# Performance work log

Measured on AMD Instinct MI355X. Metric: run time of the kernel, lower is better.

The kernel has to match this reference:

```python
import jax, jax.numpy as jnp
import numpy as np

C_Z = 128
C_H = 128
N = 768
B = 1
EPS = 1e-5


def _layer_norm(x, w, b):
    m = jnp.mean(x, axis=-1, keepdims=True)
    v = jnp.mean(jnp.square(x - m), axis=-1, keepdims=True)
    return (x - m) * jax.lax.rsqrt(v + EPS) * w + b


def setup_inputs() -> dict:
    key = jax.random.key(0)
    ks = jax.random.split(key, 12)
    s_z = 1.0 / np.sqrt(C_Z)
    s_h = 1.0 / np.sqrt(C_H)
    return {
        "z": jax.random.normal(ks[0], (B, N, N, C_Z), dtype=jnp.float32),
        "mask": jnp.ones((B, N, N), dtype=jnp.float32),
        "norm_in_weight": jnp.ones((C_Z,), dtype=jnp.float32),
        "norm_in_bias": jnp.zeros((C_Z,), dtype=jnp.float32),
        "ab_p_weight": jax.random.normal(ks[1], (2 * C_H, C_Z), dtype=jnp.float32) * s_z,
        "ab_p_bias": jnp.zeros((2 * C_H,), dtype=jnp.float32),
        "ab_g_weight": jax.random.normal(ks[2], (2 * C_H, C_Z), dtype=jnp.float32) * s_z,
        "ab_g_bias": jnp.zeros((2 * C_H,), dtype=jnp.float32),
        "g_weight": jax.random.normal(ks[3], (C_Z, C_Z), dtype=jnp.float32) * s_z,
        "g_bias": jnp.ones((C_Z,), dtype=jnp.float32),
        "norm_out_weight": jnp.ones((C_H,), dtype=jnp.float32),
        "norm_out_bias": jnp.zeros((C_H,), dtype=jnp.float32),
        "z_weight": jax.random.normal(ks[4], (C_Z, C_H), dtype=jnp.float32) * s_h,
        "z_bias": jnp.zeros((C_Z,), dtype=jnp.float32),
    }


def reference(z, mask, norm_in_weight, norm_in_bias, ab_p_weight, ab_p_bias,
              ab_g_weight, ab_g_bias, g_weight, g_bias,
              norm_out_weight, norm_out_bias, z_weight, z_bias):
    # z: [B, N, N, c_z]; mask: [B, N, N]
    zn = _layer_norm(z, norm_in_weight, norm_in_bias)
    # fused gated projection: p * sigmoid(g), masked
    p = jnp.einsum('bijc,dc->bijd', zn, ab_p_weight) + ab_p_bias
    g = jax.nn.sigmoid(jnp.einsum('bijc,dc->bijd', zn, ab_g_weight) + ab_g_bias)
    ab = p * g * mask[..., None]  # [B, N, N, 2*c_h]
    a, b = ab[..., :C_H], ab[..., C_H:]
    # outgoing triangle multiplication: sum over k of a_ik * b_jk
    x = jnp.einsum('bikc,bjkc->bijc', a, b)  # [B, N, N, c_h]
    x = _layer_norm(x, norm_out_weight, norm_out_bias)
    x = jnp.einsum('bijc,dc->bijd', x, z_weight) + z_bias  # [B, N, N, c_z]
    gate = jax.nn.sigmoid(jnp.einsum('bijc,dc->bijd', zn, g_weight) + g_bias)
    return x * gate
```

## Files before the change

### kernel.cpp

```cpp
#include <hip/hip_runtime.h>

typedef unsigned short ushort_t;
typedef __attribute__((ext_vector_type(4))) unsigned short u16x4;
typedef __attribute__((ext_vector_type(8))) unsigned short u16x8;
typedef __attribute__((ext_vector_type(2))) unsigned short u16x2;
typedef __attribute__((ext_vector_type(4))) float f32x4;
typedef __attribute__((ext_vector_type(8))) __bf16 bf16x8;

constexpr int N_ = 768;
constexpr int NN = N_ * N_;
constexpr int C  = 128;

__device__ __forceinline__ unsigned short f2bf(float f) {
  union { float f; unsigned int u; } v; v.f = f;
  unsigned int r = v.u + 0x7fffu + ((v.u >> 16) & 1u);
  return (unsigned short)(r >> 16);
}
__device__ __forceinline__ float bf2f(unsigned short u) {
  union { unsigned int i; float f; } v; v.i = ((unsigned int)u) << 16;
  return v.f;
}
__device__ __forceinline__ float sigm(float x) { return 1.f / (1.f + __expf(-x)); }

__device__ __forceinline__ void gload16(const void* g, void* l) {
  __builtin_amdgcn_global_load_lds(
      (const __attribute__((address_space(1))) unsigned int*)g,
      (__attribute__((address_space(3))) unsigned int*)l, 16, 0, 0);
}

__global__ __launch_bounds__(256) void k1_ln(const float* __restrict__ z,
                                             const float* __restrict__ w,
                                             const float* __restrict__ b,
                                             ushort_t* __restrict__ zn) {
  int row  = blockIdx.x * 4 + (threadIdx.x >> 6);
  int lane = threadIdx.x & 63;
  const float* src = z + (size_t)row * C;
  float2 v = *(const float2*)(src + lane * 2);
  float sm = v.x + v.y;
#pragma unroll
  for (int m = 1; m < 64; m <<= 1) sm += __shfl_xor(sm, m);
  float mean = sm * (1.f / 128.f);
  float d0 = v.x - mean, d1 = v.y - mean;
  float sq = d0 * d0 + d1 * d1;
#pragma unroll
  for (int m = 1; m < 64; m <<= 1) sq += __shfl_xor(sq, m);
  float rstd = rsqrtf(sq * (1.f / 128.f) + 1e-5f);
  float2 wv = *(const float2*)(w + lane * 2);
  float2 bv = *(const float2*)(b + lane * 2);
  u16x2 o; o.x = f2bf(d0 * rstd * wv.x + bv.x); o.y = f2bf(d1 * rstd * wv.y + bv.y);
  *(u16x2*)(zn + (size_t)row * C + lane * 2) = o;
}

__global__ void k0_cvt(const float* __restrict__ zw, const float* __restrict__ Wp,
                       const float* __restrict__ Wg, const float* __restrict__ Wgate,
                       ushort_t* __restrict__ zwb, ushort_t* __restrict__ Wall) {
  int i = blockIdx.x * 256 + threadIdx.x;
  if (i < 16384) zwb[i] = f2bf(zw[i]);
  if (i < 81920) {
    float v = (i < 32768) ? Wp[i] : (i < 65536 ? Wg[i - 32768] : Wgate[i - 65536]);
    Wall[i] = f2bf(v);
  }
}

constexpr int K2_ZN  = 0;
constexpr int K2_WB0 = 32768;
constexpr int K2_WB1 = 49152;
__global__ __launch_bounds__(256, 2) void k2_proj(
    const ushort_t* __restrict__ zn, const ushort_t* __restrict__ Wall,
    const float* __restrict__ bp, const float* __restrict__ bg,
    const float* __restrict__ bgate, const float* __restrict__ mask,
    ushort_t* __restrict__ a_t, ushort_t* __restrict__ b_t,
    ushort_t* __restrict__ gate_t) {
  __shared__ __align__(16) char smem[65536];
  int ij0 = blockIdx.x * 128;
  int t = threadIdx.x, lane = t & 63, wid = t >> 6;
  int rl = lane & 15, gq = lane >> 4;

  auto stage_wb = [&](int wrowbase, int wboff) {
#pragma unroll
    for (int pass = 0; pass < 4; ++pass) {
      int idx = pass * 256 + t;
      int row = idx >> 4, slot = idx & 15;
      int gcol = (slot * 16) ^ ((row & 7) << 4);
      gload16((const char*)Wall + (size_t)(wrowbase + row) * 256 + gcol,
              smem + wboff + idx * 16);
    }
  };

  {
    const char* base = (const char*)(zn + (size_t)ij0 * C);
#pragma unroll
    for (int iss = 0; iss < 8; ++iss) {
      int idx = iss * 256 + t;
      int row = idx >> 4, slot = idx & 15;
      int gcol = (slot * 16) ^ ((row & 7) << 4);
      gload16(base + row * 256 + gcol, smem + K2_ZN + idx * 16);
    }
  }
  stage_wb(0, K2_WB0);
  stage_wb(256, K2_WB1);
  __syncthreads();

  bf16x8 afr[4][2];
#pragma unroll
  for (int kk = 0; kk < 4; ++kk) {
    int kb = kk * 64 + gq * 16;
#pragma unroll
    for (int r = 0; r < 2; ++r) {
      int row = wid * 32 + r * 16 + rl;
      afr[kk][r] = *(const bf16x8*)(smem + K2_ZN + row * 256 + (kb ^ ((row & 7) << 4)));
    }
  }

  auto mfma_from = [&](f32x4 (&acc)[2][4], int wboff) {
#pragma unroll
    for (int kk = 0; kk < 4; ++kk) {
      int kb = kk * 64 + gq * 16;
      bf16x8 wf[4];
#pragma unroll
      for (int n = 0; n < 4; ++n) {
        int row = n * 16 + rl;
        wf[n] = *(const bf16x8*)(smem + wboff + row * 256 + (kb ^ ((row & 7) << 4)));
      }
#pragma unroll
      for (int r = 0; r < 2; ++r)
#pragma unroll
        for (int n = 0; n < 4; ++n)
          acc[r][n] = __builtin_amdgcn_mfma_f32_16x16x32_bf16(afr[kk][r], wf[n], acc[r][n], 0, 0, 0);
    }
  };

  auto store_epi = [&](ushort_t* dst) {
#pragma unroll
    for (int pass = 0; pass < 4; ++pass) {
      int idx = pass * 256 + t;
      int c = idx >> 4, k = idx & 15;
      u16x8 v = *(const u16x8*)(smem + c * 256 + ((k * 16) ^ ((c & 7) << 4)));
      *(u16x8*)(dst + (size_t)c * NN + k * 8) = v;
    }
  };

  for (int ci = 0; ci < 4; ++ci) {
    f32x4 accp[2][4] = {}, accg[2][4] = {};
    mfma_from(accp, K2_WB0);
    mfma_from(accg, K2_WB1);
    __syncthreads();
    stage_wb(ci < 3 ? (ci + 1) * 64 : 512, K2_WB0);
    stage_wb(ci < 3 ? 256 + (ci + 1) * 64 : 576, K2_WB1);
#pragma unroll
    for (int r = 0; r < 2; ++r) {
      int ijbase = wid * 32 + r * 16 + gq * 4;
      float4 mv = *(const float4*)(mask + ij0 + ijbase);
      float m4[4] = {mv.x, mv.y, mv.z, mv.w};
#pragma unroll
      for (int n = 0; n < 4; ++n) {
        int ch = n * 16 + rl;
        float pbv = bp[ci * 64 + ch], gbv = bg[ci * 64 + ch];
        u16x4 pk;
#pragma unroll
        for (int reg = 0; reg < 4; ++reg) {
          float pv = accp[r][n][reg] + pbv;
          float gv = sigm(accg[r][n][reg] + gbv);
          pk[reg] = f2bf(pv * gv * m4[reg]);
        }
        *(u16x4*)(smem + ch * 256 + ((ijbase * 2) ^ ((ch & 7) << 4))) = pk;
      }
    }
    __syncthreads();
    store_epi(((ci < 2) ? a_t : b_t) + (size_t)((ci & 1) * 64) * NN + ij0);
  }

  {
    f32x4 acc0[2][4] = {}, acc1[2][4] = {};
    mfma_from(acc0, K2_WB0);
    mfma_from(acc1, K2_WB1);
    __syncthreads();

    auto gate_epi = [&](f32x4 (&ag)[2][4], int hb) {
#pragma unroll
      for (int r = 0; r < 2; ++r) {
        int ijbase = wid * 32 + r * 16 + gq * 4;
#pragma unroll
        for (int n = 0; n < 4; ++n) {
          int ch = n * 16 + rl;
          float gbv = bgate[hb * 64 + ch];
          u16x4 pk;
#pragma unroll
          for (int reg = 0; reg < 4; ++reg) pk[reg] = f2bf(sigm(ag[r][n][reg] + gbv));
          *(u16x4*)(smem + ch * 256 + ((ijbase * 2) ^ ((ch & 7) << 4))) = pk;
        }
      }
    };

    gate_epi(acc0, 0);
    __syncthreads();
    store_epi(gate_t + ij0);
    __syncthreads();
    gate_epi(acc1, 1);
    __syncthreads();
    store_epi(gate_t + (size_t)64 * NN + ij0);
  }
}

__global__ __launch_bounds__(256, 2) void k3_tri(const ushort_t* __restrict__ a_t,
                                                 const ushort_t* __restrict__ b_t,
                                                 ushort_t* __restrict__ x_t) {
  __shared__ __align__(16) char smem[34816];
  int p = blockIdx.x;
  int xcd = p & 7, s = p >> 3;
  int tile = s % 36, c = xcd + 8 * (s / 36);
  int ti = tile / 6, tj = tile % 6;
  int i0 = ti * 128, j0 = tj * 128;
  const char* pa = (const char*)(a_t + (size_t)c * NN);
  const char* pb = (const char*)(b_t + (size_t)c * NN);
  int t = threadIdx.x, lane = t & 63, wid = t >> 6;
  int rl = lane & 15, gq = lane >> 4;
  int wj = (wid >> 1) * 64, wi = (wid & 1) * 64;
  f32x4 acc[4][4] = {};

  for (int ks = 0; ks < 12; ++ks) {
#pragma unroll
    for (int iss = 0; iss < 4; ++iss) {
      int idx = iss * 256 + wid * 64 + lane;
      int row = idx >> 3, slot = idx & 7;
      int gb = (slot * 16) ^ ((row & 7) << 4);
      gload16(pa + (size_t)(i0 + row) * 1536 + ks * 128 + gb,
              smem + (iss * 256 + wid * 64) * 16);
      gload16(pb + (size_t)(j0 + row) * 1536 + ks * 128 + gb,
              smem + 16384 + (iss * 256 + wid * 64) * 16);
    }
    __syncthreads();
#pragma unroll
    for (int kk = 0; kk < 2; ++kk) {
      int kb = kk * 64 + gq * 16;
      bf16x8 af[4], bf[4];
#pragma unroll
      for (int f = 0; f < 4; ++f) {
        int rowi = wi + f * 16 + rl;
        af[f] = *(const bf16x8*)(smem + rowi * 128 + (kb ^ ((rowi & 7) << 4)));
        int rowj = wj + f * 16 + rl;
        bf[f] = *(const bf16x8*)(smem + 16384 + rowj * 128 + (kb ^ ((rowj & 7) << 4)));
      }
#pragma unroll
      for (int fj = 0; fj < 4; ++fj)
#pragma unroll
        for (int fi = 0; fi < 4; ++fi)
          acc[fj][fi] = __builtin_amdgcn_mfma_f32_16x16x32_bf16(bf[fj], af[fi], acc[fj][fi], 0, 0, 0);
    }
    __syncthreads();
  }
  char* epi = smem;
#pragma unroll
  for (int fj = 0; fj < 4; ++fj) {
    int jbase = wj + fj * 16 + gq * 4;
#pragma unroll
    for (int fi = 0; fi < 4; ++fi) {
      int i = wi + fi * 16 + rl;
      u16x4 pk;
#pragma unroll
      for (int reg = 0; reg < 4; ++reg) pk[reg] = f2bf(acc[fj][fi][reg]);
      *(u16x4*)(epi + i * 272 + jbase * 2) = pk;
    }
  }
  __syncthreads();
#pragma unroll
  for (int pass = 0; pass < 8; ++pass) {
    int idx = pass * 256 + t;
    int row = idx >> 4, chunk = idx & 15;
    u16x8 v = *(const u16x8*)(epi + row * 272 + chunk * 16);
    *(u16x8*)(x_t + (size_t)c * NN + (size_t)(i0 + row) * N_ + j0 + chunk * 8) = v;
  }
}

constexpr int K4_G   = 0;
constexpr int K4_CB  = 17408;
constexpr int K4_X   = 18944;
constexpr int K4_XN  = 36352;
constexpr int K4_OUT = 18944;
__global__ __launch_bounds__(256, 2) void k4_out(
    const ushort_t* __restrict__ x_t, const ushort_t* __restrict__ gate_t,
    const float* __restrict__ wout, const float* __restrict__ bout,
    const ushort_t* __restrict__ zwb, const float* __restrict__ zbias,
    float* __restrict__ out) {
  __shared__ __align__(16) char smem[52736];
  int ij0 = blockIdx.x * 64;
  int t = threadIdx.x, lane = t & 63, wid = t >> 6;

#pragma unroll
  for (int pass = 0; pass < 4; ++pass) {
    int idx = pass * 256 + t;
    int c = idx >> 3, chunk = idx & 7;
    u16x8 vx = *(const u16x8*)(x_t + (size_t)c * NN + ij0 + chunk * 8);
    u16x4 lo, hi;
    lo[0]=vx[0]; lo[1]=vx[1]; lo[2]=vx[2]; lo[3]=vx[3];
    hi[0]=vx[4]; hi[1]=vx[5]; hi[2]=vx[6]; hi[3]=vx[7];
    *(u16x4*)(smem + K4_X + c * 136 + chunk * 16) = lo;
    *(u16x4*)(smem + K4_X + c * 136 + chunk * 16 + 8) = hi;
    u16x8 vg = *(const u16x8*)(gate_t + (size_t)c * NN + ij0 + chunk * 8);
    lo[0]=vg[0]; lo[1]=vg[1]; lo[2]=vg[2]; lo[3]=vg[3];
    hi[0]=vg[4]; hi[1]=vg[5]; hi[2]=vg[6]; hi[3]=vg[7];
    *(u16x4*)(smem + K4_G + c * 136 + chunk * 16) = lo;
    *(u16x4*)(smem + K4_G + c * 136 + chunk * 16 + 8) = hi;
  }
  if (t < 128) {
    *(float*)(smem + K4_CB + t * 4)        = zbias[t];
    *(float*)(smem + K4_CB + 512 + t * 4)  = wout[t];
    *(float*)(smem + K4_CB + 1024 + t * 4) = bout[t];
  }
  __syncthreads();

  const float* cb = (const float*)(smem + K4_CB);
#pragma unroll
  for (int q = 0; q < 16; ++q) {
    int ij = wid * 16 + q;
    float v1 = bf2f(*(const ushort_t*)(smem + K4_X + lane * 136 + ij * 2));
    float v2 = bf2f(*(const ushort_t*)(smem + K4_X + (lane + 64) * 136 + ij * 2));
    float sm = v1 + v2, sq = v1 * v1 + v2 * v2;
#pragma unroll
    for (int m = 1; m < 64; m <<= 1) { sm += __shfl_xor(sm, m); sq += __shfl_xor(sq, m); }
    float mean = sm * (1.f / 128.f);
    float var  = sq * (1.f / 128.f) - mean * mean;
    float rstd = rsqrtf(var + 1e-5f);
    float o1 = (v1 - mean) * rstd * cb[128 + lane] + cb[256 + lane];
    float o2 = (v2 - mean) * rstd * cb[128 + lane + 64] + cb[256 + lane + 64];
    *(ushort_t*)(smem + K4_XN + ij * 256 + ((lane * 2) ^ ((ij & 7) << 4))) = f2bf(o1);
    *(ushort_t*)(smem + K4_XN + ij * 256 + (((lane + 64) * 2) ^ ((ij & 7) << 4))) = f2bf(o2);
  }
  __syncthreads();

  int rl = lane & 15, gq = lane >> 4;
  int wrow = (wid >> 1) * 32, wcol = (wid & 1) * 64;
  f32x4 acc[2][4] = {};
#pragma unroll
  for (int kk = 0; kk < 4; ++kk) {
    int kb = kk * 64 + gq * 16;
    bf16x8 a[2], bfr[4];
#pragma unroll
    for (int r = 0; r < 2; ++r) {
      int row = wrow + r * 16 + rl;
      a[r] = *(const bf16x8*)(smem + K4_XN + row * 256 + (kb ^ ((row & 7) << 4)));
    }
#pragma unroll
    for (int n = 0; n < 4; ++n) {
      int d = wcol + n * 16 + rl;
      bfr[n] = *(const bf16x8*)(zwb + (size_t)d * C + kk * 32 + gq * 8);
    }
#pragma unroll
    for (int r = 0; r < 2; ++r)
#pragma unroll
      for (int n = 0; n < 4; ++n)
        acc[r][n] = __builtin_amdgcn_mfma_f32_16x16x32_bf16(a[r], bfr[n], acc[r][n], 0, 0, 0);
  }
  __syncthreads();

  float* outl = (float*)(smem + K4_OUT);
#pragma unroll
  for (int r = 0; r < 2; ++r) {
    int ijbase = wrow + r * 16 + gq * 4;
#pragma unroll
    for (int n = 0; n < 4; ++n) {
      int d = wcol + n * 16 + rl;
      float zb = cb[d];
      u16x4 gv = *(const u16x4*)(smem + K4_G + d * 136 + ijbase * 2);
#pragma unroll
      for (int reg = 0; reg < 4; ++reg)
        outl[(ijbase + reg) * 132 + d] = (acc[r][n][reg] + zb) * bf2f(gv[reg]);
    }
  }
  __syncthreads();
#pragma unroll
  for (int pass = 0; pass < 8; ++pass) {
    int idx = pass * 256 + t;
    int row = idx >> 5, ch4 = idx & 31;
    float4 v = *(const float4*)(smem + K4_OUT + row * 528 + ch4 * 16);
    *(float4*)(out + (size_t)(ij0 + row) * C + ch4 * 4) = v;
  }
}

extern "C" void kernel_launch(void* const* d_in, const int* in_sizes, int n_in,
                              void* d_out, int out_size, void* d_ws, size_t ws_size,
                              hipStream_t stream) {
  const float* z     = (const float*)d_in[0];
  const float* mask  = (const float*)d_in[1];
  const float* w_in  = (const float*)d_in[2];
  const float* b_in  = (const float*)d_in[3];
  const float* Wp    = (const float*)d_in[4];
  const float* bp    = (const float*)d_in[5];
  const float* Wg    = (const float*)d_in[6];
  const float* bg    = (const float*)d_in[7];
  const float* Wgate = (const float*)d_in[8];
  const float* bgate = (const float*)d_in[9];
  const float* w_out = (const float*)d_in[10];
  const float* b_out = (const float*)d_in[11];
  const float* zw    = (const float*)d_in[12];
  const float* zb    = (const float*)d_in[13];

  ushort_t* zwb    = (ushort_t*)d_ws;
  ushort_t* Wall   = zwb + 16384;
  ushort_t* zn     = Wall + 81920;
  ushort_t* gate_t = zn + (size_t)NN * C;
  ushort_t* a_t = (ushort_t*)d_out;
  ushort_t* b_t = a_t + (size_t)NN * C;
  float* outp = (float*)d_out;

  k1_ln<<<NN / 4, 256, 0, stream>>>(z, w_in, b_in, zn);
  k0_cvt<<<384, 256, 0, stream>>>(zw, Wp, Wg, Wgate, zwb, Wall);
  k2_proj<<<4608, 256, 0, stream>>>(zn, Wall, bp, bg, bgate, mask,
                                    a_t, b_t, gate_t);
  k3_tri<<<4608, 256, 0, stream>>>(a_t, b_t, zn );
  k4_out<<<9216, 256, 0, stream>>>(zn , gate_t, w_out, b_out, zwb, zb, outp);
}
```

Measured before the change: 687.1 us.

## Move gate projection from projection kernel into output kernel, dropping gate tensor

The gate projection (zn @ Wgate, then sigmoid) is no longer computed in k2 and written to a bf16 gate_t buffer. k4 now loads the zn tile itself and runs an extra MFMA GEMM against the bf16 gate weights, applying the sigmoid in the epilogue. This removes the write and re-read of a 768x768x128 bf16 gate tensor. In exchange, zn must be read again in k4 and x_t gets its own workspace buffer instead of reusing zn's storage.

```diff
diff --git a/kernel.cpp b/kernel.cpp
--- a/kernel.cpp
+++ b/kernel.cpp
@@ -68,9 +68,8 @@
 __global__ __launch_bounds__(256, 2) void k2_proj(
     const ushort_t* __restrict__ zn, const ushort_t* __restrict__ Wall,
     const float* __restrict__ bp, const float* __restrict__ bg,
-    const float* __restrict__ bgate, const float* __restrict__ mask,
-    ushort_t* __restrict__ a_t, ushort_t* __restrict__ b_t,
-    ushort_t* __restrict__ gate_t) {
+    const float* __restrict__ mask,
+    ushort_t* __restrict__ a_t, ushort_t* __restrict__ b_t) {
   __shared__ __align__(16) char smem[65536];
   int ij0 = blockIdx.x * 128;
   int t = threadIdx.x, lane = t & 63, wid = t >> 6;
@@ -145,8 +144,10 @@
     mfma_from(accp, K2_WB0);
     mfma_from(accg, K2_WB1);
     __syncthreads();
-    stage_wb(ci < 3 ? (ci + 1) * 64 : 512, K2_WB0);
-    stage_wb(ci < 3 ? 256 + (ci + 1) * 64 : 576, K2_WB1);
+    if (ci < 3) {
+      stage_wb((ci + 1) * 64, K2_WB0);
+      stage_wb(256 + (ci + 1) * 64, K2_WB1);
+    }
 #pragma unroll
     for (int r = 0; r < 2; ++r) {
       int ijbase = wid * 32 + r * 16 + gq * 4;
@@ -168,37 +169,6 @@
     }
     __syncthreads();
     store_epi(((ci < 2) ? a_t : b_t) + (size_t)((ci & 1) * 64) * NN + ij0);
-  }
-
-  {
-    f32x4 acc0[2][4] = {}, acc1[2][4] = {};
-    mfma_from(acc0, K2_WB0);
-    mfma_from(acc1, K2_WB1);
-    __syncthreads();
-
-    auto gate_epi = [&](f32x4 (&ag)[2][4], int hb) {
-#pragma unroll
-      for (int r = 0; r < 2; ++r) {
-        int ijbase = wid * 32 + r * 16 + gq * 4;
-#pragma unroll
-        for (int n = 0; n < 4; ++n) {
-          int ch = n * 16 + rl;
-          float gbv = bgate[hb * 64 + ch];
-          u16x4 pk;
-#pragma unroll
-          for (int reg = 0; reg < 4; ++reg) pk[reg] = f2bf(sigm(ag[r][n][reg] + gbv));
-          *(u16x4*)(smem + ch * 256 + ((ijbase * 2) ^ ((ch & 7) << 4))) = pk;
-        }
-      }
-    };
-
-    gate_epi(acc0, 0);
-    __syncthreads();
-    store_epi(gate_t + ij0);
-    __syncthreads();
-    gate_epi(acc1, 1);
-    __syncthreads();
-    store_epi(gate_t + (size_t)64 * NN + ij0);
   }
 }
 
@@ -272,20 +242,31 @@
   }
 }
 
-constexpr int K4_G   = 0;
-constexpr int K4_CB  = 17408;
-constexpr int K4_X   = 18944;
-constexpr int K4_XN  = 36352;
-constexpr int K4_OUT = 18944;
+constexpr int K4_CB  = 0;
+constexpr int K4_ZN  = 2048;
+constexpr int K4_X   = 18432;
+constexpr int K4_XN  = 35840;
+constexpr int K4_OUT = 18432;
 __global__ __launch_bounds__(256, 2) void k4_out(
-    const ushort_t* __restrict__ x_t, const ushort_t* __restrict__ gate_t,
+    const ushort_t* __restrict__ x_t, const ushort_t* __restrict__ zn,
+    const ushort_t* __restrict__ zwb, const ushort_t* __restrict__ wgateb,
     const float* __restrict__ wout, const float* __restrict__ bout,
-    const ushort_t* __restrict__ zwb, const float* __restrict__ zbias,
+    const float* __restrict__ zbias, const float* __restrict__ bgate,
     float* __restrict__ out) {
-  __shared__ __align__(16) char smem[52736];
+  __shared__ __align__(16) char smem[52224];
   int ij0 = blockIdx.x * 64;
   int t = threadIdx.x, lane = t & 63, wid = t >> 6;
 
+  {
+    const char* base = (const char*)(zn + (size_t)ij0 * C);
+#pragma unroll
+    for (int iss = 0; iss < 4; ++iss) {
+      int idx = iss * 256 + t;
+      int row = idx >> 4, slot = idx & 15;
+      int gcol = (slot * 16) ^ ((row & 7) << 4);
+      gload16(base + row * 256 + gcol, smem + K4_ZN + idx * 16);
+    }
+  }
 #pragma unroll
   for (int pass = 0; pass < 4; ++pass) {
     int idx = pass * 256 + t;
@@ -296,16 +277,12 @@
     hi[0]=vx[4]; hi[1]=vx[5]; hi[2]=vx[6]; hi[3]=vx[7];
     *(u16x4*)(smem + K4_X + c * 136 + chunk * 16) = lo;
     *(u16x4*)(smem + K4_X + c * 136 + chunk * 16 + 8) = hi;
-    u16x8 vg = *(const u16x8*)(gate_t + (size_t)c * NN + ij0 + chunk * 8);
-    lo[0]=vg[0]; lo[1]=vg[1]; lo[2]=vg[2]; lo[3]=vg[3];
-    hi[0]=vg[4]; hi[1]=vg[5]; hi[2]=vg[6]; hi[3]=vg[7];
-    *(u16x4*)(smem + K4_G + c * 136 + chunk * 16) = lo;
-    *(u16x4*)(smem + K4_G + c * 136 + chunk * 16 + 8) = hi;
   }
   if (t < 128) {
     *(float*)(smem + K4_CB + t * 4)        = zbias[t];
     *(float*)(smem + K4_CB + 512 + t * 4)  = wout[t];
     *(float*)(smem + K4_CB + 1024 + t * 4) = bout[t];
+    *(float*)(smem + K4_CB + 1536 + t * 4) = bgate[t];
   }
   __syncthreads();
 
@@ -326,10 +303,33 @@
     *(ushort_t*)(smem + K4_XN + ij * 256 + ((lane * 2) ^ ((ij & 7) << 4))) = f2bf(o1);
     *(ushort_t*)(smem + K4_XN + ij * 256 + (((lane + 64) * 2) ^ ((ij & 7) << 4))) = f2bf(o2);
   }
-  __syncthreads();
 
   int rl = lane & 15, gq = lane >> 4;
   int wrow = (wid >> 1) * 32, wcol = (wid & 1) * 64;
+
+  f32x4 acc2[2][4] = {};
+#pragma unroll
+  for (int kk = 0; kk < 4; ++kk) {
+    int kb = kk * 64 + gq * 16;
+    bf16x8 a2[2], bfr2[4];
+#pragma unroll
+    for (int r = 0; r < 2; ++r) {
+      int row = wrow + r * 16 + rl;
+      a2[r] = *(const bf16x8*)(smem + K4_ZN + row * 256 + (kb ^ ((row & 7) << 4)));
+    }
+#pragma unroll
+    for (int n = 0; n < 4; ++n) {
+      int d = wcol + n * 16 + rl;
+      bfr2[n] = *(const bf16x8*)(wgateb + (size_t)d * C + kk * 32 + gq * 8);
+    }
+#pragma unroll
+    for (int r = 0; r < 2; ++r)
+#pragma unroll
+      for (int n = 0; n < 4; ++n)
+        acc2[r][n] = __builtin_amdgcn_mfma_f32_16x16x32_bf16(a2[r], bfr2[n], acc2[r][n], 0, 0, 0);
+  }
+  __syncthreads();
+
   f32x4 acc[2][4] = {};
 #pragma unroll
   for (int kk = 0; kk < 4; ++kk) {
@@ -361,10 +361,11 @@
     for (int n = 0; n < 4; ++n) {
       int d = wcol + n * 16 + rl;
       float zb = cb[d];
-      u16x4 gv = *(const u16x4*)(smem + K4_G + d * 136 + ijbase * 2);
+      float gb = cb[384 + d];
 #pragma unroll
       for (int reg = 0; reg < 4; ++reg)
-        outl[(ijbase + reg) * 132 + d] = (acc[r][n][reg] + zb) * bf2f(gv[reg]);
+        outl[(ijbase + reg) * 132 + d] =
+            (acc[r][n][reg] + zb) * sigm(acc2[r][n][reg] + gb);
     }
   }
   __syncthreads();
@@ -395,18 +396,18 @@
   const float* zw    = (const float*)d_in[12];
   const float* zb    = (const float*)d_in[13];
 
-  ushort_t* zwb    = (ushort_t*)d_ws;
-  ushort_t* Wall   = zwb + 16384;
-  ushort_t* zn     = Wall + 81920;
-  ushort_t* gate_t = zn + (size_t)NN * C;
+  ushort_t* zwb  = (ushort_t*)d_ws;
+  ushort_t* Wall = zwb + 16384;
+  ushort_t* zn   = Wall + 81920;
+  ushort_t* x_t  = zn + (size_t)NN * C;
   ushort_t* a_t = (ushort_t*)d_out;
   ushort_t* b_t = a_t + (size_t)NN * C;
   float* outp = (float*)d_out;
 
   k1_ln<<<NN / 4, 256, 0, stream>>>(z, w_in, b_in, zn);
   k0_cvt<<<384, 256, 0, stream>>>(zw, Wp, Wg, Wgate, zwb, Wall);
-  k2_proj<<<4608, 256, 0, stream>>>(zn, Wall, bp, bg, bgate, mask,
-                                    a_t, b_t, gate_t);
-  k3_tri<<<4608, 256, 0, stream>>>(a_t, b_t, zn );
-  k4_out<<<9216, 256, 0, stream>>>(zn , gate_t, w_out, b_out, zwb, zb, outp);
-}
+  k2_proj<<<4608, 256, 0, stream>>>(zn, Wall, bp, bg, mask, a_t, b_t);
+  k3_tri<<<4608, 256, 0, stream>>>(a_t, b_t, x_t);
+  k4_out<<<9216, 256, 0, stream>>>(x_t, zn, zwb, Wall + (size_t)512 * C,
+                                   w_out, b_out, zb, bgate, outp);
+}
```

Result: faster. 668.6 us (-2.7%).
